# Optimization experiments

Measured on AMD Instinct MI355X. Metric: run time of the kernel, lower is better.

The kernel has to match this reference:

```python
import jax, jax.numpy as jnp
import numpy as np

D, H, B = 512, 8, 64
NF, NO = 16384, 8192
EPS = 1e-5


def _ln(x):
    m = jnp.mean(x, axis=-1, keepdims=True)
    v = jnp.mean((x - m) ** 2, axis=-1, keepdims=True)
    return (x - m) / jnp.sqrt(v + EPS)


def setup_inputs() -> dict:
    key = jax.random.key(0)
    ks = jax.random.split(key, 16)
    s = 1.0 / np.sqrt(D)
    inp = {
        "hf": jax.random.normal(ks[0], (NF, D), jnp.float32),
        "ho": jax.random.normal(ks[1], (NO, D), jnp.float32),
        "ps": jax.random.normal(ks[2], (B, D), jnp.float32),
        "face_batch": jnp.sort(jax.random.randint(ks[3], (NF,), 0, B)),
        "obj_batch": jnp.sort(jax.random.randint(ks[4], (NO,), 0, B)),
        "Wq": jax.random.normal(ks[5], (D, D), jnp.float32) * s,
        "bq": jnp.zeros((D,), jnp.float32),
        "Wk": jax.random.normal(ks[6], (D, D), jnp.float32) * s,
        "bk": jnp.zeros((D,), jnp.float32),
        "Wv": jax.random.normal(ks[7], (D, D), jnp.float32) * s,
        "bv": jnp.zeros((D,), jnp.float32),
        "Wo": jax.random.normal(ks[8], (D, D), jnp.float32) * s,
        "bo": jnp.zeros((D,), jnp.float32),
        "Wg": jax.random.normal(ks[9], (D, D), jnp.float32) * s,
        "bg": jnp.full((D,), -1.0, jnp.float32),  # init.constant_(bias, -1.0)
        "alpha": jax.random.normal(ks[10], (D,), jnp.float32) * 0.1,
    }
    return inp


def reference(hf, ho, ps, face_batch, obj_batch, Wq, bq, Wk, bk, Wv, bv, Wo, bo, Wg, bg, alpha):
    dh = D // H
    nodes = jnp.concatenate([hf, ho], axis=0)            # (N, D)
    seg = jnp.concatenate([face_batch, obj_batch], 0)    # (N,)
    N = nodes.shape[0]

    # single-query cross-attention done as ragged/segment attention
    # (identical math to padded MHA with key_padding_mask)
    q = (ps @ Wq + bq).reshape(B, H, dh)                 # (B, H, dh)
    k = (nodes @ Wk + bk).reshape(N, H, dh)
    v = (nodes @ Wv + bv).reshape(N, H, dh)

    scores = jnp.einsum("nhd,nhd->nh", k, q[seg]) / np.sqrt(dh)   # (N, H)
    mx = jax.ops.segment_max(scores, seg, num_segments=B)          # (B, H)
    e = jnp.exp(scores - mx[seg])                                  # (N, H)
    denom = jax.ops.segment_sum(e, seg, num_segments=B)            # (B, H)
    num = jax.ops.segment_sum(e[:, :, None] * v, seg, num_segments=B)  # (B, H, dh)
    attn = (num / denom[:, :, None]).reshape(B, D)
    attn_out = attn @ Wo + bo

    fs = _ln(ps + attn_out)                               # (B, D)
    gate = jax.nn.sigmoid(hf @ Wg + bg)                   # (NF, D)
    signal = alpha * fs[face_batch]                       # (NF, D)
    hf_new = _ln(hf + gate * signal)
    return hf_new, fs
```

## Files before the change

kernel.cpp:

```cpp
#include <hip/hip_runtime.h>
#include <hip/hip_bf16.h>
#include <math.h>

constexpr int D  = 512;
constexpr int H  = 8;
constexpr int DH = 64;
constexpr int B  = 64;
constexpr int NF = 16384;
constexpr int NO = 8192;
constexpr int NT = NF + NO;
constexpr float EPS = 1e-5f;
constexpr float LOG2E = 1.4426950408889634f;

typedef short short8 __attribute__((ext_vector_type(8)));
typedef float f32x4 __attribute__((ext_vector_type(4)));
typedef unsigned short ushort;
typedef ushort ushort8v __attribute__((ext_vector_type(8)));

__device__ __forceinline__ ushort f2bf(float f) {
  unsigned int x = __float_as_uint(f);
  x += 0x7FFF + ((x >> 16) & 1);
  return (ushort)(x >> 16);
}
__device__ __forceinline__ float bf2f(ushort u) {
  return __uint_as_float(((unsigned int)u) << 16);
}
__device__ __forceinline__ float fast_exp(float x) {
  return __builtin_amdgcn_exp2f(x * LOG2E);
}
__device__ __forceinline__ float fast_sigmoid(float z) {
  return __builtin_amdgcn_rcpf(1.0f + __builtin_amdgcn_exp2f(-z * LOG2E));
}
__device__ __forceinline__ short8 cvt8(float4 f0, float4 f1) {
  union { short8 v; __hip_bfloat162 h[4]; } u;
  u.h[0] = __float22bfloat162_rn(float2{f0.x, f0.y});
  u.h[1] = __float22bfloat162_rn(float2{f0.z, f0.w});
  u.h[2] = __float22bfloat162_rn(float2{f1.x, f1.y});
  u.h[3] = __float22bfloat162_rn(float2{f1.z, f1.w});
  return u.v;
}
__device__ __forceinline__ void gll16(const void* g, void* l) {
  __builtin_amdgcn_global_load_lds(
      (const __attribute__((address_space(1))) void*)g,
      (__attribute__((address_space(3))) void*)l, 16, 0, 0);
}

__global__ __launch_bounds__(256) void k_qproj(const float* __restrict__ ps,
                                               const float* __restrict__ Wq,
                                               const float* __restrict__ bq,
                                               float* __restrict__ q) {
  __shared__ float row[D];
  int b = blockIdx.x, cg = blockIdx.y, t = threadIdx.x;
  for (int i = t; i < D; i += 256) row[i] = ps[(size_t)b * D + i];
  __syncthreads();
  int col = cg * 64 + (t >> 2), eq = t & 3;
  float acc = 0.f;
  const float* wp = Wq + (size_t)(eq * 128) * D + col;
  #pragma unroll 8
  for (int e = 0; e < 128; ++e) acc += row[eq * 128 + e] * wp[(size_t)e * D];
  acc += __shfl_xor(acc, 1); acc += __shfl_xor(acc, 2);
  if (eq == 0) q[(size_t)b * D + col] = acc + bq[col];
}

__global__ __launch_bounds__(256) void k_pkproj(const float* __restrict__ q,
                                                const float* __restrict__ Wk,
                                                const float* __restrict__ bk,
                                                float* __restrict__ Pk,
                                                float* __restrict__ qbk) {
  int b = blockIdx.x, h = blockIdx.y;
  __shared__ float qs[DH];
  __shared__ float bks[DH];
  int t = threadIdx.x;
  if (t < DH) { qs[t] = q[b * D + h * DH + t]; bks[t] = bk[h * DH + t]; }
  __syncthreads();
  for (int e = t; e < D; e += 256) {
    float acc = 0.f;
    #pragma unroll 8
    for (int j = 0; j < DH; ++j) acc += Wk[(size_t)e * D + h * DH + j] * qs[j];
    Pk[((size_t)b * H + h) * D + e] = acc;
  }
  if (t == 0) {
    float s = 0.f;
    for (int j = 0; j < DH; ++j) s += bks[j] * qs[j];
    qbk[b * H + h] = s;
  }
}

__global__ void k_bounds(const int* __restrict__ fb, const int* __restrict__ ob,
                         int* __restrict__ fstart, int* __restrict__ ostart) {
  int t = threadIdx.x;
  if (t <= B) {
    int lo = 0, hi = NF;
    while (lo < hi) { int mid = (lo + hi) >> 1; if (fb[mid] < t) lo = mid + 1; else hi = mid; }
    fstart[t] = lo;
  } else if (t >= 128 && t <= 128 + B) {
    int v = t - 128;
    int lo = 0, hi = NO;
    while (lo < hi) { int mid = (lo + hi) >> 1; if (ob[mid] < v) lo = mid + 1; else hi = mid; }
    ostart[v] = lo;
  }
}

__global__ __launch_bounds__(256) void k_prepW(const float* __restrict__ Wg,
                                               ushort* __restrict__ Wgt) {
  __shared__ float tile[32][33];
  int bx = blockIdx.x, by = blockIdx.y;
  int tx = threadIdx.x & 31, ty = threadIdx.x >> 5;
  #pragma unroll
  for (int i = 0; i < 4; ++i)
    tile[ty + i * 8][tx] = Wg[(size_t)(by * 32 + ty + i * 8) * D + bx * 32 + tx];
  __syncthreads();
  #pragma unroll
  for (int i = 0; i < 4; ++i)
    Wgt[(size_t)(bx * 32 + ty + i * 8) * D + by * 32 + tx] = f2bf(tile[tx][ty + i * 8]);
}

__global__ __launch_bounds__(256) void k_gate(const float* __restrict__ hf,
                                              const ushort* __restrict__ Wgt,
                                              const float* __restrict__ bg,
                                              ushort* __restrict__ gateb) {
  __shared__ float  Asf[2][4096];
  __shared__ ushort Bs[2][4096];
  const int tid = threadIdx.x, lane = tid & 63, w = tid >> 6;
  const int rowBase = blockIdx.x * 128, colBase = blockIdx.y * 128;
  const int wm = w >> 1, wn = w & 1;
  const int lrow = lane & 15, kg = lane >> 4;

  int ra[4], ca[4];
  #pragma unroll
  for (int j = 0; j < 4; ++j) {
    int ia = (w * 4 + j) * 64 + lane;
    ra[j] = ia >> 3;
    ca[j] = (ia & 7) ^ (ra[j] & 7);
  }
  int cb[2], cc[2];
  #pragma unroll
  for (int j = 0; j < 2; ++j) {
    int ib = (w * 2 + j) * 64 + lane;
    cb[j] = ib >> 2;
    cc[j] = (ib & 3) ^ ((cb[j] >> 1) & 3);
  }

#define STAGE(buf, k0)                                                          \
  {                                                                             \
    _Pragma("unroll")                                                           \
    for (int j = 0; j < 4; ++j)                                                 \
      gll16(hf + (size_t)(rowBase + ra[j]) * D + (k0) + ca[j] * 4,              \
            &Asf[buf][(w * 4 + j) * 256]);                                      \
    _Pragma("unroll")                                                           \
    for (int j = 0; j < 2; ++j)                                                 \
      gll16(Wgt + (size_t)(colBase + cb[j]) * D + (k0) + cc[j] * 8,             \
            &Bs[buf][(w * 2 + j) * 512]);                                       \
  }

  STAGE(0, 0);
  __syncthreads();

  f32x4 acc[4][4] = {};
  for (int t = 0; t < 16; ++t) {
    const int cur = t & 1;
    if (t < 15) STAGE(cur ^ 1, (t + 1) * 32);
    short8 av[4], bv[4];
    #pragma unroll
    for (int m = 0; m < 4; ++m) {
      const int a_r = wm * 64 + m * 16 + lrow;
      const float* Ab = &Asf[cur][a_r * 32];
      const int c0 = (2 * kg) ^ (a_r & 7), c1 = (2 * kg + 1) ^ (a_r & 7);
      av[m] = cvt8(*(const float4*)(Ab + c0 * 4), *(const float4*)(Ab + c1 * 4));
    }
    #pragma unroll
    for (int n = 0; n < 4; ++n) {
      const int b_c = wn * 64 + n * 16 + lrow;
      bv[n] = *(const short8*)&Bs[cur][b_c * 32 + (kg ^ ((b_c >> 1) & 3)) * 8];
    }
    #pragma unroll
    for (int m = 0; m < 4; ++m)
      #pragma unroll
      for (int n = 0; n < 4; ++n)
        acc[m][n] = __builtin_amdgcn_mfma_f32_16x16x32_bf16(av[m], bv[n], acc[m][n], 0, 0, 0);
    __syncthreads();
  }
#undef STAGE

  #pragma unroll
  for (int n = 0; n < 4; ++n) {
    const int col = colBase + wn * 64 + n * 16 + lrow;
    const float bgv = bg[col];
    #pragma unroll
    for (int m = 0; m < 4; ++m) {
      const int row0 = rowBase + wm * 64 + m * 16 + kg * 4;
      #pragma unroll
      for (int r = 0; r < 4; ++r)
        gateb[(size_t)(row0 + r) * D + col] = f2bf(fast_sigmoid(acc[m][n][r] + bgv));
    }
  }
}

__global__ __launch_bounds__(256) void k_scores(const float* __restrict__ hf,
                                                const float* __restrict__ ho,
                                                const int* __restrict__ fb,
                                                const int* __restrict__ ob,
                                                const float* __restrict__ Pk,
                                                const float* __restrict__ qbk,
                                                float* __restrict__ scores) {
  int lane = threadIdx.x & 63;
  int n = blockIdx.x * 4 + (threadIdx.x >> 6);
  int b; const float* row;
  if (n < NF) { b = fb[n]; row = hf + (size_t)n * D; }
  else        { b = ob[n - NF]; row = ho + (size_t)(n - NF) * D; }
  const float4* r4 = (const float4*)row;
  float4 x0 = r4[lane * 2], x1 = r4[lane * 2 + 1];
  float acc[H];
  #pragma unroll
  for (int h = 0; h < H; ++h) {
    const float4* p4 = (const float4*)(Pk + ((size_t)b * H + h) * D) + lane * 2;
    float4 p0 = p4[0], p1 = p4[1];
    acc[h] = x0.x * p0.x + x0.y * p0.y + x0.z * p0.z + x0.w * p0.w +
             x1.x * p1.x + x1.y * p1.y + x1.z * p1.z + x1.w * p1.w;
  }
  #pragma unroll
  for (int h = 0; h < H; ++h) {
    float v = acc[h];
    #pragma unroll
    for (int off = 32; off; off >>= 1) v += __shfl_xor(v, off);
    if (lane == h) scores[(size_t)n * H + h] = (v + qbk[b * H + h]) * 0.125f;
  }
}

__global__ __launch_bounds__(512) void k_segsoftmax(const float* __restrict__ scores,
                                                    const int* __restrict__ fstart,
                                                    const int* __restrict__ ostart,
                                                    float* __restrict__ evals,
                                                    float* __restrict__ denom) {
  int b = blockIdx.x;
  int h = threadIdx.x >> 6, lane = threadIdx.x & 63;
  int f0 = fstart[b], f1 = fstart[b + 1];
  int o0 = ostart[b], o1 = ostart[b + 1];
  float m = -1e30f;
  for (int i = f0 + lane; i < f1; i += 64) m = fmaxf(m, scores[(size_t)i * H + h]);
  for (int i = o0 + lane; i < o1; i += 64) m = fmaxf(m, scores[(size_t)(NF + i) * H + h]);
  #pragma unroll
  for (int off = 32; off; off >>= 1) m = fmaxf(m, __shfl_xor(m, off));
  float s = 0.f;
  for (int i = f0 + lane; i < f1; i += 64) {
    float e = fast_exp(scores[(size_t)i * H + h] - m);
    evals[(size_t)i * H + h] = e; s += e;
  }
  for (int i = o0 + lane; i < o1; i += 64) {
    float e = fast_exp(scores[(size_t)(NF + i) * H + h] - m);
    evals[(size_t)(NF + i) * H + h] = e; s += e;
  }
  #pragma unroll
  for (int off = 32; off; off >>= 1) s += __shfl_xor(s, off);
  if (lane == 0) denom[b * H + h] = s;
}

__global__ __launch_bounds__(512) void k_Taccum(const float* __restrict__ hf,
                                                const float* __restrict__ ho,
                                                const int* __restrict__ fstart,
                                                const int* __restrict__ ostart,
                                                const float* __restrict__ evals,
                                                float* __restrict__ T8) {
  int b = blockIdx.x, chunk = blockIdx.y;
  int e = threadIdx.x;
  int f0 = fstart[b], flen = fstart[b + 1] - f0;
  int o0 = ostart[b], olen = ostart[b + 1] - o0;
  int L = flen + olen;
  float acc[8] = {0.f, 0.f, 0.f, 0.f, 0.f, 0.f, 0.f, 0.f};
  for (int idx = chunk; idx < L; idx += 8) {
    int n; const float* row;
    if (idx < flen) { n = f0 + idx; row = hf + (size_t)n * D; }
    else            { n = NF + o0 + (idx - flen); row = ho + (size_t)(o0 + idx - flen) * D; }
    float x = row[e];
    const float4* ev = (const float4*)(evals + (size_t)n * H);
    float4 e0 = ev[0], e1 = ev[1];
    acc[0] += e0.x * x; acc[1] += e0.y * x; acc[2] += e0.z * x; acc[3] += e0.w * x;
    acc[4] += e1.x * x; acc[5] += e1.y * x; acc[6] += e1.z * x; acc[7] += e1.w * x;
  }
  #pragma unroll
  for (int h = 0; h < H; ++h)
    T8[(((size_t)chunk * B + b) * H + h) * D + e] = acc[h];
}

__global__ __launch_bounds__(256) void k_attn(const float* __restrict__ T8,
                                              const float* __restrict__ denom,
                                              const float* __restrict__ Wv,
                                              const float* __restrict__ bv,
                                              float* __restrict__ attn) {
  __shared__ float Ts[D];
  int b = blockIdx.x, h = blockIdx.y, t = threadIdx.x;
  for (int i = t; i < D; i += 256) {
    float s = 0.f;
    #pragma unroll
    for (int c2 = 0; c2 < 8; ++c2)
      s += T8[(((size_t)c2 * B + b) * H + h) * D + i];
    Ts[i] = s;
  }
  __syncthreads();
  int col = h * DH + (t >> 2), eq = t & 3;
  float acc = 0.f;
  const float* wp = Wv + (size_t)(eq * 128) * D + col;
  #pragma unroll 8
  for (int e = 0; e < 128; ++e) acc += Ts[eq * 128 + e] * wp[(size_t)e * D];
  acc += __shfl_xor(acc, 1); acc += __shfl_xor(acc, 2);
  if (eq == 0) attn[(size_t)b * D + col] = acc / denom[b * H + h] + bv[col];
}

__global__ __launch_bounds__(256) void k_x(const float* __restrict__ attn,
                                           const float* __restrict__ Wo,
                                           const float* __restrict__ bo,
                                           const float* __restrict__ ps,
                                           float* __restrict__ x) {
  __shared__ float As[D];
  int b = blockIdx.x, cg = blockIdx.y, t = threadIdx.x;
  for (int i = t; i < D; i += 256) As[i] = attn[(size_t)b * D + i];
  __syncthreads();
  int col = cg * 64 + (t >> 2), eq = t & 3;
  float acc = 0.f;
  const float* wp = Wo + (size_t)(eq * 128) * D + col;
  #pragma unroll 8
  for (int e = 0; e < 128; ++e) acc += As[eq * 128 + e] * wp[(size_t)e * D];
  acc += __shfl_xor(acc, 1); acc += __shfl_xor(acc, 2);
  if (eq == 0) x[(size_t)b * D + col] = acc + bo[col] + ps[(size_t)b * D + col];
}

__global__ __launch_bounds__(512) void k_ln(const float* __restrict__ x,
                                            float* __restrict__ fs) {
  __shared__ float redS[8], redQ[8];
  __shared__ float sM, sI;
  int b = blockIdx.x, t = threadIdx.x;
  float v = x[(size_t)b * D + t];
  float s = v, sq = v * v;
  #pragma unroll
  for (int off = 32; off; off >>= 1) { s += __shfl_xor(s, off); sq += __shfl_xor(sq, off); }
  int wv = t >> 6, ln = t & 63;
  if (ln == 0) { redS[wv] = s; redQ[wv] = sq; }
  __syncthreads();
  if (t == 0) {
    float S = 0.f, Q = 0.f;
    #pragma unroll
    for (int i = 0; i < 8; ++i) { S += redS[i]; Q += redQ[i]; }
    float mean = S * (1.f / D);
    float var = Q * (1.f / D) - mean * mean;
    sM = mean; sI = rsqrtf(var + EPS);
  }
  __syncthreads();
  fs[(size_t)b * D + t] = (v - sM) * sI;
}

__global__ __launch_bounds__(256) void k_final(const float* __restrict__ hf,
                                               const ushort* __restrict__ gateb,
                                               const float* __restrict__ alpha,
                                               const float* __restrict__ fs,
                                               const int* __restrict__ fb,
                                               float* __restrict__ out) {
  const int w = threadIdx.x >> 6, lane = threadIdx.x & 63;
  const int row = blockIdx.x * 4 + w;
  const int b = fb[row];
  const float* hr = hf + (size_t)row * D + lane * 8;
  const ushort* gr = gateb + (size_t)row * D + lane * 8;
  const float* fr = fs + (size_t)b * D + lane * 8;
  const float* ar = alpha + lane * 8;
  float4 h0 = *(const float4*)hr, h1 = *(const float4*)(hr + 4);
  union { ushort8v v; ushort u[8]; } ug;
  ug.v = *(const ushort8v*)gr;
  float4 p0 = *(const float4*)fr, p1 = *(const float4*)(fr + 4);
  float4 a0 = *(const float4*)ar, a1 = *(const float4*)(ar + 4);
  float hv[8] = {h0.x, h0.y, h0.z, h0.w, h1.x, h1.y, h1.z, h1.w};
  float pv[8] = {p0.x, p0.y, p0.z, p0.w, p1.x, p1.y, p1.z, p1.w};
  float av[8] = {a0.x, a0.y, a0.z, a0.w, a1.x, a1.y, a1.z, a1.w};
  float x[8], s = 0.f, sq = 0.f;
  #pragma unroll
  for (int i = 0; i < 8; ++i) {
    x[i] = hv[i] + bf2f(ug.u[i]) * (av[i] * pv[i]);
    s += x[i]; sq += x[i] * x[i];
  }
  #pragma unroll
  for (int off = 32; off; off >>= 1) { s += __shfl_xor(s, off); sq += __shfl_xor(sq, off); }
  float mean = s * (1.f / D);
  float inv = rsqrtf(sq * (1.f / D) - mean * mean + EPS);
  float* op = out + (size_t)row * D + lane * 8;
  float4 o0 = {(x[0] - mean) * inv, (x[1] - mean) * inv, (x[2] - mean) * inv, (x[3] - mean) * inv};
  float4 o1 = {(x[4] - mean) * inv, (x[5] - mean) * inv, (x[6] - mean) * inv, (x[7] - mean) * inv};
  *(float4*)op = o0;
  *(float4*)(op + 4) = o1;
}

extern "C" void kernel_launch(void* const* d_in, const int* in_sizes, int n_in,
                              void* d_out, int out_size, void* d_ws, size_t ws_size,
                              hipStream_t stream) {
  const float* hf    = (const float*)d_in[0];
  const float* ho    = (const float*)d_in[1];
  const float* ps    = (const float*)d_in[2];
  const int*   fb    = (const int*)d_in[3];
  const int*   ob    = (const int*)d_in[4];
  const float* Wq    = (const float*)d_in[5];
  const float* bq    = (const float*)d_in[6];
  const float* Wk    = (const float*)d_in[7];
  const float* bk    = (const float*)d_in[8];
  const float* Wv    = (const float*)d_in[9];
  const float* bv    = (const float*)d_in[10];
  const float* Wo    = (const float*)d_in[11];
  const float* bo    = (const float*)d_in[12];
  const float* Wg    = (const float*)d_in[13];
  const float* bg    = (const float*)d_in[14];
  const float* alpha = (const float*)d_in[15];

  float* out    = (float*)d_out;
  float* fs_out = out + (size_t)NF * D;

  ushort* Wgt   = (ushort*)d_ws;
  ushort* gateb = Wgt + 512 * 512;
  float* fbase  = (float*)(gateb + (size_t)NF * D);
  float* q      = fbase;
  float* Pk     = q + B * D;
  float* qbk    = Pk + B * H * D;
  float* scores = qbk + B * H;
  float* evals  = scores + (size_t)NT * H;
  float* denom  = evals + (size_t)NT * H;
  float* T8     = denom + B * H;
  float* attn   = T8 + (size_t)8 * B * H * D;
  float* xbuf   = attn + B * D;
  int* fstart   = (int*)(xbuf + B * D);
  int* ostart   = fstart + (B + 1);

  k_prepW<<<dim3(16, 16), 256, 0, stream>>>(Wg, Wgt);
  k_qproj<<<dim3(B, 8), 256, 0, stream>>>(ps, Wq, bq, q);
  k_pkproj<<<dim3(B, H), 256, 0, stream>>>(q, Wk, bk, Pk, qbk);
  k_bounds<<<1, 256, 0, stream>>>(fb, ob, fstart, ostart);
  k_gate<<<dim3(NF / 128, 4), 256, 0, stream>>>(hf, Wgt, bg, gateb);
  k_scores<<<NT / 4, 256, 0, stream>>>(hf, ho, fb, ob, Pk, qbk, scores);
  k_segsoftmax<<<B, 512, 0, stream>>>(scores, fstart, ostart, evals, denom);
  k_Taccum<<<dim3(B, 8), 512, 0, stream>>>(hf, ho, fstart, ostart, evals, T8);
  k_attn<<<dim3(B, H), 256, 0, stream>>>(T8, denom, Wv, bv, attn);
  k_x<<<dim3(B, 8), 256, 0, stream>>>(attn, Wo, bo, ps, xbuf);
  k_ln<<<B, 512, 0, stream>>>(xbuf, fs_out);
  k_final<<<NF / 4, 256, 0, stream>>>(hf, gateb, alpha, fs_out, fb, out);
}
```

Before: 147.5 us.

## Pre-convert node features to bf16 and merge small prep kernels into one launch

Four small setup kernels (Q projection, Pk projection, segment bounds, Wg transpose) are folded into one multi-role prep kernel. The same launch also converts all hf/ho rows to a bf16 copy. The gate GEMM, score and T-accumulation kernels then read the bf16 copy instead of fp32, which halves their global reads and drops in-loop conversion in the gate GEMM. In exchange there is an extra full read and write of the node matrix in the prep pass, plus reduced precision in the scores and attention accumulation.

```diff
diff --git a/kernel.cpp b/kernel.cpp
--- a/kernel.cpp
+++ b/kernel.cpp
@@ -12,6 +12,13 @@
 constexpr float EPS = 1e-5f;
 constexpr float LOG2E = 1.4426950408889634f;
 
+constexpr int PREP_PK   = 512;
+constexpr int PREP_BND  = PREP_PK;
+constexpr int PREP_WG0  = PREP_BND + 1;
+constexpr int PREP_CVT0 = PREP_WG0 + 256;
+constexpr int CVT_BLOCKS = NT * D / 2048;
+constexpr int PREP_TOTAL = PREP_CVT0 + CVT_BLOCKS;
+
 typedef short short8 __attribute__((ext_vector_type(8)));
 typedef float f32x4 __attribute__((ext_vector_type(4)));
 typedef unsigned short ushort;
@@ -45,108 +52,108 @@
       (__attribute__((address_space(3))) void*)l, 16, 0, 0);
 }
 
-__global__ __launch_bounds__(256) void k_qproj(const float* __restrict__ ps,
-                                               const float* __restrict__ Wq,
-                                               const float* __restrict__ bq,
-                                               float* __restrict__ q) {
-  __shared__ float row[D];
-  int b = blockIdx.x, cg = blockIdx.y, t = threadIdx.x;
-  for (int i = t; i < D; i += 256) row[i] = ps[(size_t)b * D + i];
-  __syncthreads();
-  int col = cg * 64 + (t >> 2), eq = t & 3;
-  float acc = 0.f;
-  const float* wp = Wq + (size_t)(eq * 128) * D + col;
-  #pragma unroll 8
-  for (int e = 0; e < 128; ++e) acc += row[eq * 128 + e] * wp[(size_t)e * D];
-  acc += __shfl_xor(acc, 1); acc += __shfl_xor(acc, 2);
-  if (eq == 0) q[(size_t)b * D + col] = acc + bq[col];
-}
-
-__global__ __launch_bounds__(256) void k_pkproj(const float* __restrict__ q,
-                                                const float* __restrict__ Wk,
-                                                const float* __restrict__ bk,
-                                                float* __restrict__ Pk,
-                                                float* __restrict__ qbk) {
-  int b = blockIdx.x, h = blockIdx.y;
-  __shared__ float qs[DH];
-  __shared__ float bks[DH];
-  int t = threadIdx.x;
-  if (t < DH) { qs[t] = q[b * D + h * DH + t]; bks[t] = bk[h * DH + t]; }
-  __syncthreads();
-  for (int e = t; e < D; e += 256) {
-    float acc = 0.f;
-    #pragma unroll 8
-    for (int j = 0; j < DH; ++j) acc += Wk[(size_t)e * D + h * DH + j] * qs[j];
-    Pk[((size_t)b * H + h) * D + e] = acc;
-  }
-  if (t == 0) {
-    float s = 0.f;
-    for (int j = 0; j < DH; ++j) s += bks[j] * qs[j];
-    qbk[b * H + h] = s;
-  }
-}
-
-__global__ void k_bounds(const int* __restrict__ fb, const int* __restrict__ ob,
-                         int* __restrict__ fstart, int* __restrict__ ostart) {
-  int t = threadIdx.x;
-  if (t <= B) {
-    int lo = 0, hi = NF;
-    while (lo < hi) { int mid = (lo + hi) >> 1; if (fb[mid] < t) lo = mid + 1; else hi = mid; }
-    fstart[t] = lo;
-  } else if (t >= 128 && t <= 128 + B) {
-    int v = t - 128;
-    int lo = 0, hi = NO;
-    while (lo < hi) { int mid = (lo + hi) >> 1; if (ob[mid] < v) lo = mid + 1; else hi = mid; }
-    ostart[v] = lo;
-  }
-}
-
-__global__ __launch_bounds__(256) void k_prepW(const float* __restrict__ Wg,
-                                               ushort* __restrict__ Wgt) {
-  __shared__ float tile[32][33];
-  int bx = blockIdx.x, by = blockIdx.y;
-  int tx = threadIdx.x & 31, ty = threadIdx.x >> 5;
-  #pragma unroll
-  for (int i = 0; i < 4; ++i)
-    tile[ty + i * 8][tx] = Wg[(size_t)(by * 32 + ty + i * 8) * D + bx * 32 + tx];
-  __syncthreads();
-  #pragma unroll
-  for (int i = 0; i < 4; ++i)
-    Wgt[(size_t)(bx * 32 + ty + i * 8) * D + by * 32 + tx] = f2bf(tile[tx][ty + i * 8]);
-}
-
-__global__ __launch_bounds__(256) void k_gate(const float* __restrict__ hf,
+__global__ __launch_bounds__(256) void k_prep(const float* __restrict__ ps,
+                                              const float* __restrict__ Wq,
+                                              const float* __restrict__ bq,
+                                              const float* __restrict__ Wk,
+                                              const float* __restrict__ bk,
+                                              const float* __restrict__ Wg,
+                                              const float* __restrict__ hf,
+                                              const float* __restrict__ ho,
+                                              const int* __restrict__ fb,
+                                              const int* __restrict__ ob,
+                                              float* __restrict__ Pk,
+                                              float* __restrict__ qbk,
+                                              ushort* __restrict__ Wgt,
+                                              ushort* __restrict__ nodesb,
+                                              int* __restrict__ fstart,
+                                              int* __restrict__ ostart) {
+  __shared__ float shm[1056];
+  const int bid = blockIdx.x, t = threadIdx.x;
+  if (bid < PREP_PK) {
+    const int b = bid >> 3, h = bid & 7;
+    for (int i = t; i < D; i += 256) shm[i] = ps[(size_t)b * D + i];
+    __syncthreads();
+    {
+      const int j = t >> 2, eq = t & 3;
+      const int col = h * 64 + j;
+      float acc = 0.f;
+      const float* wp = Wq + (size_t)(eq * 128) * D + col;
+      #pragma unroll 8
+      for (int e = 0; e < 128; ++e) acc += shm[eq * 128 + e] * wp[(size_t)e * D];
+      acc += __shfl_xor(acc, 1); acc += __shfl_xor(acc, 2);
+      if (eq == 0) shm[512 + j] = acc + bq[col];
+    }
+    __syncthreads();
+    for (int e = t; e < D; e += 256) {
+      float acc = 0.f;
+      #pragma unroll 8
+      for (int j = 0; j < DH; ++j) acc += Wk[(size_t)e * D + h * DH + j] * shm[512 + j];
+      Pk[((size_t)b * H + h) * D + e] = acc;
+    }
+    if (t == 0) {
+      float s = 0.f;
+      for (int j = 0; j < DH; ++j) s += bk[h * DH + j] * shm[512 + j];
+      qbk[b * H + h] = s;
+    }
+  } else if (bid == PREP_BND) {
+    if (t <= B) {
+      int lo = 0, hi = NF;
+      while (lo < hi) { int mid = (lo + hi) >> 1; if (fb[mid] < t) lo = mid + 1; else hi = mid; }
+      fstart[t] = lo;
+    } else if (t >= 128 && t <= 128 + B) {
+      int v = t - 128;
+      int lo = 0, hi = NO;
+      while (lo < hi) { int mid = (lo + hi) >> 1; if (ob[mid] < v) lo = mid + 1; else hi = mid; }
+      ostart[v] = lo;
+    }
+  } else if (bid < PREP_CVT0) {
+    float (*tile)[33] = (float(*)[33])shm;
+    const int tb = bid - PREP_WG0;
+    const int bx = tb & 15, by = tb >> 4;
+    const int tx = t & 31, ty = t >> 5;
+    #pragma unroll
+    for (int i = 0; i < 4; ++i)
+      tile[ty + i * 8][tx] = Wg[(size_t)(by * 32 + ty + i * 8) * D + bx * 32 + tx];
+    __syncthreads();
+    #pragma unroll
+    for (int i = 0; i < 4; ++i)
+      Wgt[(size_t)(bx * 32 + ty + i * 8) * D + by * 32 + tx] = f2bf(tile[tx][ty + i * 8]);
+  } else {
+    size_t idx = (size_t)(bid - PREP_CVT0) * 2048 + (size_t)t * 8;
+    const float* src = (idx < (size_t)NF * D) ? (hf + idx) : (ho + (idx - (size_t)NF * D));
+    float4 f0 = *(const float4*)src, f1 = *(const float4*)(src + 4);
+    *(short8*)(nodesb + idx) = cvt8(f0, f1);
+  }
+}
+
+__global__ __launch_bounds__(256) void k_gate(const ushort* __restrict__ hfb,
                                               const ushort* __restrict__ Wgt,
                                               const float* __restrict__ bg,
                                               ushort* __restrict__ gateb) {
-  __shared__ float  Asf[2][4096];
+  __shared__ ushort Asb[2][4096];
   __shared__ ushort Bs[2][4096];
   const int tid = threadIdx.x, lane = tid & 63, w = tid >> 6;
   const int rowBase = blockIdx.x * 128, colBase = blockIdx.y * 128;
   const int wm = w >> 1, wn = w & 1;
   const int lrow = lane & 15, kg = lane >> 4;
 
-  int ra[4], ca[4];
-  #pragma unroll
-  for (int j = 0; j < 4; ++j) {
-    int ia = (w * 4 + j) * 64 + lane;
-    ra[j] = ia >> 3;
-    ca[j] = (ia & 7) ^ (ra[j] & 7);
-  }
-  int cb[2], cc[2];
+  int ra[2], ca[2], cb[2], cc[2];
   #pragma unroll
   for (int j = 0; j < 2; ++j) {
-    int ib = (w * 2 + j) * 64 + lane;
-    cb[j] = ib >> 2;
-    cc[j] = (ib & 3) ^ ((cb[j] >> 1) & 3);
+    int ia = (w * 2 + j) * 64 + lane;
+    ra[j] = ia >> 2;
+    ca[j] = (ia & 3) ^ ((ra[j] >> 1) & 3);
+    cb[j] = ra[j];
+    cc[j] = ca[j];
   }
 
 #define STAGE(buf, k0)                                                          \
   {                                                                             \
     _Pragma("unroll")                                                           \
-    for (int j = 0; j < 4; ++j)                                                 \
-      gll16(hf + (size_t)(rowBase + ra[j]) * D + (k0) + ca[j] * 4,              \
-            &Asf[buf][(w * 4 + j) * 256]);                                      \
+    for (int j = 0; j < 2; ++j)                                                 \
+      gll16(hfb + (size_t)(rowBase + ra[j]) * D + (k0) + ca[j] * 8,             \
+            &Asb[buf][(w * 2 + j) * 512]);                                      \
     _Pragma("unroll")                                                           \
     for (int j = 0; j < 2; ++j)                                                 \
       gll16(Wgt + (size_t)(colBase + cb[j]) * D + (k0) + cc[j] * 8,             \
@@ -164,9 +171,7 @@
     #pragma unroll
     for (int m = 0; m < 4; ++m) {
       const int a_r = wm * 64 + m * 16 + lrow;
-      const float* Ab = &Asf[cur][a_r * 32];
-      const int c0 = (2 * kg) ^ (a_r & 7), c1 = (2 * kg + 1) ^ (a_r & 7);
-      av[m] = cvt8(*(const float4*)(Ab + c0 * 4), *(const float4*)(Ab + c1 * 4));
+      av[m] = *(const short8*)&Asb[cur][a_r * 32 + (kg ^ ((a_r >> 1) & 3)) * 8];
     }
     #pragma unroll
     for (int n = 0; n < 4; ++n) {
@@ -196,8 +201,7 @@
   }
 }
 
-__global__ __launch_bounds__(256) void k_scores(const float* __restrict__ hf,
-                                                const float* __restrict__ ho,
+__global__ __launch_bounds__(256) void k_scores(const ushort* __restrict__ nodesb,
                                                 const int* __restrict__ fb,
                                                 const int* __restrict__ ob,
                                                 const float* __restrict__ Pk,
@@ -205,18 +209,19 @@
                                                 float* __restrict__ scores) {
   int lane = threadIdx.x & 63;
   int n = blockIdx.x * 4 + (threadIdx.x >> 6);
-  int b; const float* row;
-  if (n < NF) { b = fb[n]; row = hf + (size_t)n * D; }
-  else        { b = ob[n - NF]; row = ho + (size_t)(n - NF) * D; }
-  const float4* r4 = (const float4*)row;
-  float4 x0 = r4[lane * 2], x1 = r4[lane * 2 + 1];
+  int b = (n < NF) ? fb[n] : ob[n - NF];
+  union { short8 v; ushort u[8]; } ux;
+  ux.v = *(const short8*)(nodesb + (size_t)n * D + lane * 8);
+  float xf[8];
+  #pragma unroll
+  for (int i = 0; i < 8; ++i) xf[i] = bf2f(ux.u[i]);
   float acc[H];
   #pragma unroll
   for (int h = 0; h < H; ++h) {
     const float4* p4 = (const float4*)(Pk + ((size_t)b * H + h) * D) + lane * 2;
     float4 p0 = p4[0], p1 = p4[1];
-    acc[h] = x0.x * p0.x + x0.y * p0.y + x0.z * p0.z + x0.w * p0.w +
-             x1.x * p1.x + x1.y * p1.y + x1.z * p1.z + x1.w * p1.w;
+    acc[h] = xf[0] * p0.x + xf[1] * p0.y + xf[2] * p0.z + xf[3] * p0.w +
+             xf[4] * p1.x + xf[5] * p1.y + xf[6] * p1.z + xf[7] * p1.w;
   }
   #pragma unroll
   for (int h = 0; h < H; ++h) {
@@ -255,8 +260,7 @@
   if (lane == 0) denom[b * H + h] = s;
 }
 
-__global__ __launch_bounds__(512) void k_Taccum(const float* __restrict__ hf,
-                                                const float* __restrict__ ho,
+__global__ __launch_bounds__(512) void k_Taccum(const ushort* __restrict__ nodesb,
                                                 const int* __restrict__ fstart,
                                                 const int* __restrict__ ostart,
                                                 const float* __restrict__ evals,
@@ -268,10 +272,8 @@
   int L = flen + olen;
   float acc[8] = {0.f, 0.f, 0.f, 0.f, 0.f, 0.f, 0.f, 0.f};
   for (int idx = chunk; idx < L; idx += 8) {
-    int n; const float* row;
-    if (idx < flen) { n = f0 + idx; row = hf + (size_t)n * D; }
-    else            { n = NF + o0 + (idx - flen); row = ho + (size_t)(o0 + idx - flen) * D; }
-    float x = row[e];
+    int n = (idx < flen) ? (f0 + idx) : (NF + o0 + (idx - flen));
+    float x = bf2f(nodesb[(size_t)n * D + e]);
     const float4* ev = (const float4*)(evals + (size_t)n * H);
     float4 e0 = ev[0], e1 = ev[1];
     acc[0] += e0.x * x; acc[1] += e0.y * x; acc[2] += e0.z * x; acc[3] += e0.w * x;
@@ -409,11 +411,11 @@
   float* out    = (float*)d_out;
   float* fs_out = out + (size_t)NF * D;
 
-  ushort* Wgt   = (ushort*)d_ws;
-  ushort* gateb = Wgt + 512 * 512;
-  float* fbase  = (float*)(gateb + (size_t)NF * D);
-  float* q      = fbase;
-  float* Pk     = q + B * D;
+  ushort* Wgt    = (ushort*)d_ws;
+  ushort* gateb  = Wgt + 512 * 512;
+  ushort* nodesb = gateb + (size_t)NF * D;
+  float* fbase   = (float*)(nodesb + (size_t)NT * D);
+  float* Pk     = fbase;
   float* qbk    = Pk + B * H * D;
   float* scores = qbk + B * H;
   float* evals  = scores + (size_t)NT * H;
@@ -424,14 +426,12 @@
   int* fstart   = (int*)(xbuf + B * D);
   int* ostart   = fstart + (B + 1);
 
-  k_prepW<<<dim3(16, 16), 256, 0, stream>>>(Wg, Wgt);
-  k_qproj<<<dim3(B, 8), 256, 0, stream>>>(ps, Wq, bq, q);
-  k_pkproj<<<dim3(B, H), 256, 0, stream>>>(q, Wk, bk, Pk, qbk);
-  k_bounds<<<1, 256, 0, stream>>>(fb, ob, fstart, ostart);
-  k_gate<<<dim3(NF / 128, 4), 256, 0, stream>>>(hf, Wgt, bg, gateb);
-  k_scores<<<NT / 4, 256, 0, stream>>>(hf, ho, fb, ob, Pk, qbk, scores);
+  k_prep<<<PREP_TOTAL, 256, 0, stream>>>(ps, Wq, bq, Wk, bk, Wg, hf, ho, fb, ob,
+                                         Pk, qbk, Wgt, nodesb, fstart, ostart);
+  k_gate<<<dim3(NF / 128, 4), 256, 0, stream>>>(nodesb, Wgt, bg, gateb);
+  k_scores<<<NT / 4, 256, 0, stream>>>(nodesb, fb, ob, Pk, qbk, scores);
   k_segsoftmax<<<B, 512, 0, stream>>>(scores, fstart, ostart, evals, denom);
-  k_Taccum<<<dim3(B, 8), 512, 0, stream>>>(hf, ho, fstart, ostart, evals, T8);
+  k_Taccum<<<dim3(B, 8), 512, 0, stream>>>(nodesb, fstart, ostart, evals, T8);
   k_attn<<<dim3(B, H), 256, 0, stream>>>(T8, denom, Wv, bv, attn);
   k_x<<<dim3(B, 8), 256, 0, stream>>>(attn, Wo, bo, ps, xbuf);
   k_ln<<<B, 512, 0, stream>>>(xbuf, fs_out);
```

New measurement: 131.5 us. 1.12x faster.
